# Kernel tuning notes

Hardware: AMD Instinct MI355X
Metric: run time of the kernel (lower is better)

## Reference

```python
import math
import jax
import jax.numpy as jnp
import numpy as np

N_IMG = 8
A = 3
H = 100
W = 100
STRIDE = 16
IMG = 1600
PRE_NMS_TOP_N = 2000
POST_NMS_TOP_N = 1000
NMS_THRESH = 0.7
MIN_SIZE = 0
BBOX_XFORM_CLIP = math.log(1000.0 / 16.0)


def setup_inputs() -> dict:
    key = jax.random.key(0)
    k1, k2 = jax.random.split(key)
    objectness = jax.random.normal(k1, (N_IMG, A, H, W), jnp.float32)
    box_regression = jax.random.normal(k2, (N_IMG, A * 4, H, W), jnp.float32) * 0.5
    # Grid anchors, flattened in (H, W, A) order to match objectness.permute(0,2,3,1)
    cy = (jnp.arange(H, dtype=jnp.float32) + 0.5) * STRIDE  # [H]
    cx = (jnp.arange(W, dtype=jnp.float32) + 0.5) * STRIDE  # [W]
    half = jnp.array([64.0, 128.0, 256.0], jnp.float32) / 2.0  # [A]
    cy = cy[:, None, None]  # [H,1,1]
    cx = cx[None, :, None]  # [1,W,1]
    s = half[None, None, :]  # [1,1,A]
    x1, y1, x2, y2 = jnp.broadcast_arrays(cx - s, cy - s, cx + s, cy + s)
    anc = jnp.stack([x1, y1, x2, y2], axis=-1).reshape(-1, 4)  # [H*W*A, 4]
    anchors = jnp.broadcast_to(anc[None], (N_IMG, H * W * A, 4)).copy()
    return {
        "objectness": objectness,
        "box_regression": box_regression,
        "anchors": anchors,
        "image_height": IMG,
        "image_width": IMG,
    }


def _decode(deltas, boxes):
    # BoxCoder(weights=(1,1,1,1)).decode with TO_REMOVE=1
    widths = boxes[..., 2] - boxes[..., 0] + 1.0
    heights = boxes[..., 3] - boxes[..., 1] + 1.0
    ctr_x = boxes[..., 0] + 0.5 * widths
    ctr_y = boxes[..., 1] + 0.5 * heights
    dx, dy = deltas[..., 0], deltas[..., 1]
    dw = jnp.minimum(deltas[..., 2], BBOX_XFORM_CLIP)
    dh = jnp.minimum(deltas[..., 3], BBOX_XFORM_CLIP)
    pcx = dx * widths + ctr_x
    pcy = dy * heights + ctr_y
    pw = jnp.exp(dw) * widths
    ph = jnp.exp(dh) * heights
    return jnp.stack(
        [pcx - 0.5 * pw, pcy - 0.5 * ph, pcx + 0.5 * pw - 1.0, pcy + 0.5 * ph - 1.0],
        axis=-1,
    )


def _nms_keep(boxes, valid, thresh):
    # boxes [n,4] sorted by descending score; valid: pre-filter mask.
    n = boxes.shape[0]
    x1, y1, x2, y2 = boxes[:, 0], boxes[:, 1], boxes[:, 2], boxes[:, 3]
    areas = (x2 - x1 + 1.0) * (y2 - y1 + 1.0)
    xx1 = jnp.maximum(x1[:, None], x1[None, :])
    yy1 = jnp.maximum(y1[:, None], y1[None, :])
    xx2 = jnp.minimum(x2[:, None], x2[None, :])
    yy2 = jnp.minimum(y2[:, None], y2[None, :])
    inter = jnp.maximum(xx2 - xx1 + 1.0, 0.0) * jnp.maximum(yy2 - yy1 + 1.0, 0.0)
    iou = inter / (areas[:, None] + areas[None, :] - inter)
    idx = jnp.arange(n)

    def body(i, keep):
        sup = keep[i] & (iou[i] > thresh) & (idx > i)
        return keep & ~sup

    return jax.lax.fori_loop(0, n, body, valid)


def _forward(objectness, box_regression, anchors, image_height, image_width):
    N, A_, H_, W_ = objectness.shape
    scores = jax.nn.sigmoid(objectness.transpose(0, 2, 3, 1).reshape(N, -1))  # [N, A*H*W]
    deltas = (
        box_regression.reshape(N, A_, 4, H_, W_)
        .transpose(0, 3, 4, 1, 2)
        .reshape(N, -1, 4)
    )
    pre = min(PRE_NMS_TOP_N, scores.shape[1])
    top_scores, top_idx = jax.lax.top_k(scores, pre)  # sorted descending
    deltas = jnp.take_along_axis(deltas, top_idx[:, :, None], axis=1)
    anc = jnp.take_along_axis(anchors, top_idx[:, :, None], axis=1)
    props = _decode(deltas, anc)  # [N, pre, 4]
    # clip to image (fact = 1)
    xs = jnp.clip(props[..., 0::2], 0.0, image_width - 1.0)
    ys = jnp.clip(props[..., 1::2], 0.0, image_height - 1.0)
    props = jnp.stack([xs[..., 0], ys[..., 0], xs[..., 1], ys[..., 1]], axis=-1)
    # filter small / out-of-image-center boxes
    ws = props[..., 2] - props[..., 0] + 1.0
    hs = props[..., 3] - props[..., 1] + 1.0
    xc = props[..., 0] + ws / 2.0
    yc = props[..., 1] + hs / 2.0
    valid = (ws >= MIN_SIZE) & (hs >= MIN_SIZE) & (xc < image_width) & (yc < image_height)
    keep = jax.vmap(lambda b, v: _nms_keep(b, v, NMS_THRESH))(props, valid)

    def _select(b, s, k):
        # compact kept boxes (already score-sorted) into fixed-size output
        rank = jnp.cumsum(k) - 1
        tgt = jnp.where(k & (rank < POST_NMS_TOP_N), rank, POST_NMS_TOP_N)
        ob = jnp.zeros((POST_NMS_TOP_N + 1, 4), b.dtype).at[tgt].set(b)[:POST_NMS_TOP_N]
        os = jnp.zeros((POST_NMS_TOP_N + 1,), s.dtype).at[tgt].set(s)[:POST_NMS_TOP_N]
        ov = jnp.arange(POST_NMS_TOP_N) < jnp.minimum(jnp.sum(k), POST_NMS_TOP_N)
        return ob, os, ov

    return jax.vmap(_select)(props, top_scores, keep)


def reference(objectness, box_regression, anchors, image_height, image_width):
    # Returns (boxes [N,post,4], objectness scores [N,post], valid mask [N,post])
    return _forward(objectness, box_regression, anchors, image_height, image_width)
```

## Files before the change

### kernel.cpp

```cpp
#include <hip/hip_runtime.h>
#include <math.h>
#include <stdint.h>

#define NIMG   8
#define NA     30000
#define PRE_N  2000
#define POST_N 1000
#define NMS_TH 0.7f
#define DCLIP  4.135166556742356f
#define IMGF   1600.0f
#define IMGM1  1599.0f
#define CAND_MAX 4096


__global__ __launch_bounds__(1024) void topk_decode(
    const float* __restrict__ obj, const float* __restrict__ breg,
    float* __restrict__ wsBoxes, float* __restrict__ wsScores,
    int* __restrict__ wsValid)
{
    const int n    = blockIdx.x;
    const int tid  = threadIdx.x;
    const int lane = tid & 63;
    const int wid  = tid >> 6;

    __shared__ unsigned int   hist[4096];
    __shared__ unsigned short sufx[4096];
    __shared__ uint64_t       grp[CAND_MAX];
    __shared__ unsigned int   wsum[16];
    __shared__ unsigned int   sbstar;

    for (int b = tid; b < 4096; b += 1024) hist[b] = 0u;
    __syncthreads();

    const float* objn = obj + n * NA;

    for (int j = tid; j < NA; j += 1024) {
        unsigned int u = __float_as_uint(objn[j]);
        unsigned int k = (u & 0x80000000u) ? ~u : (u | 0x80000000u);
        atomicAdd(&hist[k >> 20], 1u);
    }
    __syncthreads();

    unsigned int c0 = hist[tid*4+0], c1 = hist[tid*4+1],
                 c2 = hist[tid*4+2], c3 = hist[tid*4+3];
    unsigned int p = c0 + c1 + c2 + c3;
    unsigned int s = p;
    #pragma unroll
    for (int off = 1; off < 64; off <<= 1) {
        unsigned int v = __shfl_down(s, off);
        if (lane + off < 64) s += v;
    }
    if (lane == 0) wsum[wid] = s;
    __syncthreads();
    unsigned int wafter = 0;
    for (int w = wid + 1; w < 16; ++w) wafter += wsum[w];
    unsigned int after = (s - p) + wafter;
    {
        unsigned int S3 = after + c3;
        unsigned int S2 = S3 + c2;
        unsigned int S1 = S2 + c1;
        unsigned int S0 = S1 + c0;
        if (S3 >= PRE_N && after < PRE_N) { sbstar = tid*4+3; }
        if (S2 >= PRE_N && S3    < PRE_N) { sbstar = tid*4+2; }
        if (S1 >= PRE_N && S2    < PRE_N) { sbstar = tid*4+1; }
        if (S0 >= PRE_N && S1    < PRE_N) { sbstar = tid*4+0; }
        sufx[tid*4+0] = (unsigned short)S1;
        sufx[tid*4+1] = (unsigned short)S2;
        sufx[tid*4+2] = (unsigned short)S3;
        sufx[tid*4+3] = (unsigned short)after;
    }
    hist[tid*4+0] = 0u; hist[tid*4+1] = 0u;
    hist[tid*4+2] = 0u; hist[tid*4+3] = 0u;
    __syncthreads();
    const unsigned int bstar = sbstar;

    for (int j = tid; j < NA; j += 1024) {
        unsigned int u = __float_as_uint(objn[j]);
        unsigned int k = (u & 0x80000000u) ? ~u : (u | 0x80000000u);
        unsigned int b = k >> 20;
        if (b < bstar) continue;
        int a = j / 10000, t = j - a * 10000;
        uint64_t key = (((uint64_t)(~k)) << 32) | (unsigned int)(t * 3 + a);
        unsigned int slot = (unsigned int)sufx[b] + atomicAdd(&hist[b], 1u);
        if (slot < CAND_MAX) grp[slot] = key;
    }
    __syncthreads();

    const unsigned int total =
        min((unsigned int)sufx[bstar] + hist[bstar], (unsigned int)CAND_MAX);

    for (unsigned int slot = tid; slot < total; slot += 1024) {
        const uint64_t key = grp[slot];
        const unsigned int hi = (unsigned int)(key >> 32);
        const unsigned int b  = 4095u - (hi >> 20);
        const unsigned int gbeg = sufx[b];
        const unsigned int gend =
            min(gbeg + hist[b], (unsigned int)CAND_MAX);
        unsigned int rank = gbeg;
        unsigned int g = gbeg;
        for (; g + 8u <= gend; g += 8u) {
            uint64_t v0 = grp[g+0], v1 = grp[g+1], v2 = grp[g+2], v3 = grp[g+3];
            uint64_t v4 = grp[g+4], v5 = grp[g+5], v6 = grp[g+6], v7 = grp[g+7];
            unsigned int r0 = (v0 < key) ? 1u : 0u;
            r0 += (v1 < key) ? 1u : 0u;
            r0 += (v2 < key) ? 1u : 0u;
            r0 += (v3 < key) ? 1u : 0u;
            r0 += (v4 < key) ? 1u : 0u;
            r0 += (v5 < key) ? 1u : 0u;
            r0 += (v6 < key) ? 1u : 0u;
            r0 += (v7 < key) ? 1u : 0u;
            rank += r0;
        }
        for (; g < gend; ++g)
            rank += (grp[g] < key) ? 1u : 0u;
        if (rank >= PRE_N) continue;

        unsigned int idx = (unsigned int)key;
        unsigned int k   = ~hi;
        unsigned int u   = (k & 0x80000000u) ? (k & 0x7fffffffu) : ~k;
        float logit = __uint_as_float(u);
        float score = 1.0f / (1.0f + expf(-logit));

        int a = idx % 3, t = idx / 3, w = t % 100, h = t / 100;
        const float* bp = breg + n*120000 + (a*4)*10000 + t;
        float dx = bp[0], dy = bp[10000], dw = bp[20000], dh = bp[30000];

        float half = (a == 0) ? 32.0f : ((a == 1) ? 64.0f : 128.0f);
        float cx = w * 16.0f + 8.0f, cy = h * 16.0f + 8.0f;
        float x1 = cx - half, y1 = cy - half, x2 = cx + half, y2 = cy + half;
        float wd = x2 - x1 + 1.0f, hg = y2 - y1 + 1.0f;
        float cxr = x1 + 0.5f * wd, cyr = y1 + 0.5f * hg;
        dw = fminf(dw, DCLIP); dh = fminf(dh, DCLIP);
        float pcx = dx * wd + cxr, pcy = dy * hg + cyr;
        float pw = expf(dw) * wd, ph = expf(dh) * hg;
        float px1 = pcx - 0.5f * pw, py1 = pcy - 0.5f * ph;
        float px2 = pcx + 0.5f * pw - 1.0f, py2 = pcy + 0.5f * ph - 1.0f;
        px1 = fminf(fmaxf(px1, 0.0f), IMGM1);
        px2 = fminf(fmaxf(px2, 0.0f), IMGM1);
        py1 = fminf(fmaxf(py1, 0.0f), IMGM1);
        py2 = fminf(fmaxf(py2, 0.0f), IMGM1);
        float wss = px2 - px1 + 1.0f, hss = py2 - py1 + 1.0f;
        float xc = px1 + wss * 0.5f, yc = py1 + hss * 0.5f;
        int valid = (wss >= 0.0f) && (hss >= 0.0f) && (xc < IMGF) && (yc < IMGF);

        ((float4*)wsBoxes)[n * PRE_N + (int)rank] = make_float4(px1, py1, px2, py2);
        wsScores[n * PRE_N + (int)rank] = score;
        wsValid [n * PRE_N + (int)rank] = valid;
    }
}

__global__ __launch_bounds__(512) void nms_mask(
    const float* __restrict__ wsBoxes, uint64_t* __restrict__ mask)
{
    const int blk  = blockIdx.x;
    const int n    = blk >> 5;
    const int i_t  = blk & 31;
    const int tid  = threadIdx.x;
    const int lane = tid & 63;
    const int wv   = tid >> 6;

    __shared__ uint64_t tile[64 * 33];

    for (int idx = tid; idx < 64 * 33; idx += 512) tile[idx] = 0ull;
    __syncthreads();

    const int r = i_t * 64 + lane;
    float4 rb = (r < PRE_N) ? ((const float4*)wsBoxes)[n * PRE_N + r]
                            : make_float4(0.f, 0.f, 0.f, 0.f);
    float ra = (rb.z - rb.x + 1.0f) * (rb.w - rb.y + 1.0f);

    for (int j_t = i_t + wv; j_t < 32; j_t += 8) {
        const int j = j_t * 64 + lane;
        float4 cb = (j < PRE_N) ? ((const float4*)wsBoxes)[n * PRE_N + j]
                                : make_float4(3e30f, 3e30f, 3e30f, 3e30f);
        float ca = (cb.z - cb.x + 1.0f) * (cb.w - cb.y + 1.0f);
        const uint64_t jmask = (j_t == 31) ? 0xFFFFull : ~0ull;
        const bool diag = (j_t == i_t);
        uint64_t myword = 0ull;

        #pragma unroll
        for (int c = 0; c < 64; ++c) {
            float rx1 = __int_as_float(__builtin_amdgcn_readlane(__float_as_int(rb.x), c));
            float ry1 = __int_as_float(__builtin_amdgcn_readlane(__float_as_int(rb.y), c));
            float rx2 = __int_as_float(__builtin_amdgcn_readlane(__float_as_int(rb.z), c));
            float ry2 = __int_as_float(__builtin_amdgcn_readlane(__float_as_int(rb.w), c));
            float rar = __int_as_float(__builtin_amdgcn_readlane(__float_as_int(ra), c));
            float xx1 = fmaxf(rx1, cb.x), yy1 = fmaxf(ry1, cb.y);
            float xx2 = fminf(rx2, cb.z), yy2 = fminf(ry2, cb.w);
            float ww = fmaxf(xx2 - xx1 + 1.0f, 0.0f);
            float hh = fmaxf(yy2 - yy1 + 1.0f, 0.0f);
            float inter = ww * hh;
            float denom = rar + ca - inter;
            unsigned long long bits = __ballot(inter > NMS_TH * denom) & jmask;
            if (diag) bits &= (c == 63) ? 0ull : ((~0ull) << (c + 1));
            if (lane == c) myword = bits;
        }
        tile[lane * 33 + j_t] = myword;
    }
    __syncthreads();

    uint64_t* mrow = mask + ((size_t)n * PRE_N + (size_t)i_t * 64) * 32;
    const int cmax = (i_t == 31) ? 16 : 64;
    for (int idx = tid; idx < cmax * 32; idx += 512) {
        const int rr = idx >> 5, w = idx & 31;
        mrow[idx] = tile[rr * 33 + w];
    }
}

#define SL(n,b) \
    "global_load_dword v" #n ", %[voff], %[sbase]\n\t" \
    "v_add_u32 %[voff], 0x100, %[voff]\n\t"

#define SS(n,b) \
    "s_waitcnt vmcnt(63)\n\t" \
    "v_readlane_b32 %[t], v" #n ", %[lw]\n\t" \
    "s_bitcmp1_b32 %[win], " #b "\n\t" \
    "s_cselect_b32 %[m], 0, -1\n\t" \
    "s_sub_i32 %[kept], %[kept], %[m]\n\t" \
    "s_and_b32 %[t], %[t], %[m]\n\t" \
    "s_or_b32 %[win], %[win], %[t]\n\t" \
    "v_and_b32 v" #n ", %[m], v" #n "\n\t" \
    "v_or_b32 %[rem], %[rem], v" #n "\n\t" \
    "global_load_dword v" #n ", %[voff], %[sbase]\n\t" \
    "v_add_u32 %[voff], 0x100, %[voff]\n\t"

#define SN(n,b,w) \
    "s_waitcnt vmcnt(" #w ")\n\t" \
    "v_readlane_b32 %[t], v" #n ", %[lw]\n\t" \
    "s_bitcmp1_b32 %[win], " #b "\n\t" \
    "s_cselect_b32 %[m], 0, -1\n\t" \
    "s_sub_i32 %[kept], %[kept], %[m]\n\t" \
    "s_and_b32 %[t], %[t], %[m]\n\t" \
    "s_or_b32 %[win], %[win], %[t]\n\t" \
    "v_and_b32 v" #n ", %[m], v" #n "\n\t" \
    "v_or_b32 %[rem], %[rem], v" #n "\n\t"

#define SWIN \
    "s_add_u32 %[lw], %[lw], 1\n\t" \
    "v_readlane_b32 %[t], %[rem], %[lw]\n\t" \
    "s_mov_b32 %[win], %[t]\n\t"

#define ROW_A(M) M(64,0) M(65,1) M(66,2) M(67,3) M(68,4) M(69,5) M(70,6) M(71,7) \
    M(72,8) M(73,9) M(74,10) M(75,11) M(76,12) M(77,13) M(78,14) M(79,15) \
    M(80,16) M(81,17) M(82,18) M(83,19) M(84,20) M(85,21) M(86,22) M(87,23) \
    M(88,24) M(89,25) M(90,26) M(91,27) M(92,28) M(93,29) M(94,30) M(95,31)
#define ROW_B(M) M(96,0) M(97,1) M(98,2) M(99,3) M(100,4) M(101,5) M(102,6) M(103,7) \
    M(104,8) M(105,9) M(106,10) M(107,11) M(108,12) M(109,13) M(110,14) M(111,15) \
    M(112,16) M(113,17) M(114,18) M(115,19) M(116,20) M(117,21) M(118,22) M(119,23) \
    M(120,24) M(121,25) M(122,26) M(123,27) M(124,28) M(125,29) M(126,30) M(127,31)

__global__ __launch_bounds__(256) void nms_scan_select(
    const float* __restrict__ wsBoxes, const float* __restrict__ wsScores,
    const int* __restrict__ wsValid, const uint64_t* __restrict__ mask,
    float* __restrict__ out)
{
    const int n   = blockIdx.x;
    const int tid = threadIdx.x;

    __shared__ __align__(8) unsigned char invb[256];
    __shared__ unsigned int keepw32[64];
    __shared__ int sscan[256];

    unsigned int byte = 0xFFu;
    if (tid < PRE_N / 8) {
        byte = 0u;
        for (int q = 0; q < 8; ++q)
            byte |= (wsValid[n * PRE_N + tid * 8 + q] ? 0u : 1u) << q;
    }
    invb[tid] = (unsigned char)byte;
    __syncthreads();

    if (tid < 64) {
        unsigned int rem = ((const unsigned int*)invb)[tid];
        unsigned long long sbase =
            (unsigned long long)(const void*)(mask + (size_t)n * PRE_N * 32);
        unsigned int voff = (unsigned int)(tid * 4);
        int win_, m_, t_, lw_, kept_, cnt_;

        asm volatile(
            "s_waitcnt vmcnt(0) lgkmcnt(0)\n\t"
            "s_mov_b32 %[kept], 0\n\t"
            "s_mov_b32 %[lw], 0\n\t"
            ROW_A(SL) ROW_B(SL)
            "v_readlane_b32 %[t], %[rem], %[lw]\n\t"
            "s_mov_b32 %[win], %[t]\n\t"
            "s_mov_b32 %[cnt], 30\n\t"
            "Lnms_%=:\n\t"
            ROW_A(SS)
            SWIN
            ROW_B(SS)
            SWIN
            "s_cmp_ge_i32 %[kept], 0x3e8\n\t"
            "s_cbranch_scc1 Lend_%=\n\t"
            "s_sub_u32 %[cnt], %[cnt], 1\n\t"
            "s_cmp_lg_u32 %[cnt], 0\n\t"
            "s_cbranch_scc1 Lnms_%=\n\t"
            SS(64,0) SS(65,1) SS(66,2) SS(67,3) SS(68,4) SS(69,5) SS(70,6) SS(71,7)
            SS(72,8) SS(73,9) SS(74,10) SS(75,11) SS(76,12) SS(77,13) SS(78,14) SS(79,15)
            SN(80,16,63) SN(81,17,62) SN(82,18,61) SN(83,19,60)
            SN(84,20,59) SN(85,21,58) SN(86,22,57) SN(87,23,56)
            SN(88,24,55) SN(89,25,54) SN(90,26,53) SN(91,27,52)
            SN(92,28,51) SN(93,29,50) SN(94,30,49) SN(95,31,48)
            SWIN
            SN(96,0,47) SN(97,1,46) SN(98,2,45) SN(99,3,44)
            SN(100,4,43) SN(101,5,42) SN(102,6,41) SN(103,7,40)
            SN(104,8,39) SN(105,9,38) SN(106,10,37) SN(107,11,36)
            SN(108,12,35) SN(109,13,34) SN(110,14,33) SN(111,15,32)
            SN(112,16,31) SN(113,17,30) SN(114,18,29) SN(115,19,28)
            SN(116,20,27) SN(117,21,26) SN(118,22,25) SN(119,23,24)
            SN(120,24,23) SN(121,25,22) SN(122,26,21) SN(123,27,20)
            SN(124,28,19) SN(125,29,18) SN(126,30,17) SN(127,31,16)
            SWIN
            SN(64,0,15) SN(65,1,14) SN(66,2,13) SN(67,3,12)
            SN(68,4,11) SN(69,5,10) SN(70,6,9) SN(71,7,8)
            SN(72,8,7) SN(73,9,6) SN(74,10,5) SN(75,11,4)
            SN(76,12,3) SN(77,13,2) SN(78,14,1) SN(79,15,0)
            "Lend_%=:\n\t"
            "s_waitcnt vmcnt(0)\n\t"
            : [rem]"+v"(rem), [voff]"+v"(voff),
              [win]"=&s"(win_), [m]"=&s"(m_), [t]"=&s"(t_),
              [lw]"=&s"(lw_), [kept]"=&s"(kept_), [cnt]"=&s"(cnt_)
            : [sbase]"s"(sbase)
            : "scc", "vcc", "memory",
              "v64","v65","v66","v67","v68","v69","v70","v71",
              "v72","v73","v74","v75","v76","v77","v78","v79",
              "v80","v81","v82","v83","v84","v85","v86","v87",
              "v88","v89","v90","v91","v92","v93","v94","v95",
              "v96","v97","v98","v99","v100","v101","v102","v103",
              "v104","v105","v106","v107","v108","v109","v110","v111",
              "v112","v113","v114","v115","v116","v117","v118","v119",
              "v120","v121","v122","v123","v124","v125","v126","v127");

        keepw32[tid] = ~rem;
    }
    __syncthreads();

    int c[8]; const int base8 = tid * 8;
    int lsum = 0;
    for (int q = 0; q < 8; ++q) {
        const int i = base8 + q;
        c[q] = (i < PRE_N) ? (int)((keepw32[i >> 5] >> (i & 31)) & 1u) : 0;
        lsum += c[q];
    }
    sscan[tid] = lsum;
    __syncthreads();
    for (int off = 1; off < 256; off <<= 1) {
        int v = (tid >= off) ? sscan[tid - off] : 0;
        __syncthreads();
        sscan[tid] += v;
        __syncthreads();
    }
    const int excl  = sscan[tid] - lsum;
    const int total = sscan[255];

    float* ob  = out + n * POST_N * 4;
    float* osc = out + NIMG * POST_N * 4 + n * POST_N;
    float* ovd = out + NIMG * POST_N * 5 + n * POST_N;

    for (int i = tid; i < POST_N * 4; i += 256) ob[i] = 0.0f;
    for (int i = tid; i < POST_N; i += 256) osc[i] = 0.0f;
    const int lim = min(total, POST_N);
    for (int i = tid; i < POST_N; i += 256) ovd[i] = (i < lim) ? 1.0f : 0.0f;
    __syncthreads();

    int run = excl;
    for (int q = 0; q < 8; ++q) {
        const int i = base8 + q;
        if (i < PRE_N && c[q]) {
            if (run < POST_N) {
                float4 b = ((const float4*)wsBoxes)[n * PRE_N + i];
                ob[run * 4 + 0] = b.x;
                ob[run * 4 + 1] = b.y;
                ob[run * 4 + 2] = b.z;
                ob[run * 4 + 3] = b.w;
                osc[run] = wsScores[n * PRE_N + i];
            }
            run++;
        }
    }
}

extern "C" void kernel_launch(void* const* d_in, const int* in_sizes, int n_in,
                              void* d_out, int out_size, void* d_ws, size_t ws_size,
                              hipStream_t stream) {
    const float* obj  = (const float*)d_in[0];
    const float* breg = (const float*)d_in[1];
    float* ws        = (float*)d_ws;
    float* wsBoxes   = ws;
    float* wsScores  = ws + 64000;
    int*   wsValid   = (int*)(ws + 80000);
    uint64_t* wsMask = (uint64_t*)(ws + 96000);

    topk_decode<<<NIMG, 1024, 0, stream>>>(obj, breg, wsBoxes, wsScores, wsValid);
    nms_mask<<<NIMG * 32, 512, 0, stream>>>(wsBoxes, wsMask);
    nms_scan_select<<<NIMG, 256, 0, stream>>>(wsBoxes, wsScores, wsValid, wsMask,
                                              (float*)d_out);
}
```

Measured before the change: 176.2 us.

## Add second-level radix split for oversized histogram bins in top-k ranking

Bins holding more than 64 candidates are subdivided by a second 12-bit radix histogram and scatter into a secondary buffer, so each element's rank comes from comparing only within its small sub-bin instead of scanning the whole large bin. This targets the quadratic rank computation in dense bins near the top of normal-distributed logits. It adds extra shared memory (another histogram, suffix array and candidate buffer) and several block-wide barriers per large bin, which may lower occupancy and add serial overhead.

```diff
diff --git a/kernel.cpp b/kernel.cpp
--- a/kernel.cpp
+++ b/kernel.cpp
@@ -11,7 +11,46 @@
 #define IMGF   1600.0f
 #define IMGM1  1599.0f
 #define CAND_MAX 4096
-
+#define BIG_BIN  64
+
+
+__device__ __forceinline__ void decode_store(
+    uint64_t key, unsigned int rank, int n, const float* __restrict__ breg,
+    float* __restrict__ wsBoxes, float* __restrict__ wsScores,
+    int* __restrict__ wsValid)
+{
+    unsigned int idx = (unsigned int)key;
+    unsigned int k   = ~((unsigned int)(key >> 32));
+    unsigned int u   = (k & 0x80000000u) ? (k & 0x7fffffffu) : ~k;
+    float logit = __uint_as_float(u);
+    float score = 1.0f / (1.0f + expf(-logit));
+
+    int a = idx % 3, t = idx / 3, w = t % 100, h = t / 100;
+    const float* bp = breg + n*120000 + (a*4)*10000 + t;
+    float dx = bp[0], dy = bp[10000], dw = bp[20000], dh = bp[30000];
+
+    float half = (a == 0) ? 32.0f : ((a == 1) ? 64.0f : 128.0f);
+    float cx = w * 16.0f + 8.0f, cy = h * 16.0f + 8.0f;
+    float x1 = cx - half, y1 = cy - half, x2 = cx + half, y2 = cy + half;
+    float wd = x2 - x1 + 1.0f, hg = y2 - y1 + 1.0f;
+    float cxr = x1 + 0.5f * wd, cyr = y1 + 0.5f * hg;
+    dw = fminf(dw, DCLIP); dh = fminf(dh, DCLIP);
+    float pcx = dx * wd + cxr, pcy = dy * hg + cyr;
+    float pw = expf(dw) * wd, ph = expf(dh) * hg;
+    float px1 = pcx - 0.5f * pw, py1 = pcy - 0.5f * ph;
+    float px2 = pcx + 0.5f * pw - 1.0f, py2 = pcy + 0.5f * ph - 1.0f;
+    px1 = fminf(fmaxf(px1, 0.0f), IMGM1);
+    px2 = fminf(fmaxf(px2, 0.0f), IMGM1);
+    py1 = fminf(fmaxf(py1, 0.0f), IMGM1);
+    py2 = fminf(fmaxf(py2, 0.0f), IMGM1);
+    float wss = px2 - px1 + 1.0f, hss = py2 - py1 + 1.0f;
+    float xc = px1 + wss * 0.5f, yc = py1 + hss * 0.5f;
+    int valid = (wss >= 0.0f) && (hss >= 0.0f) && (xc < IMGF) && (yc < IMGF);
+
+    ((float4*)wsBoxes)[n * PRE_N + (int)rank] = make_float4(px1, py1, px2, py2);
+    wsScores[n * PRE_N + (int)rank] = score;
+    wsValid [n * PRE_N + (int)rank] = valid;
+}
 
 __global__ __launch_bounds__(1024) void topk_decode(
     const float* __restrict__ obj, const float* __restrict__ breg,
@@ -26,10 +65,16 @@
     __shared__ unsigned int   hist[4096];
     __shared__ unsigned short sufx[4096];
     __shared__ uint64_t       grp[CAND_MAX];
+    __shared__ unsigned int   hist2[4096];
+    __shared__ unsigned short sufx2[4096];
+    __shared__ uint64_t       grp2[CAND_MAX];
     __shared__ unsigned int   wsum[16];
     __shared__ unsigned int   sbstar;
+    __shared__ int            lbin[64];
+    __shared__ unsigned int   lbcnt;
 
     for (int b = tid; b < 4096; b += 1024) hist[b] = 0u;
+    if (tid == 0) lbcnt = 0u;
     __syncthreads();
 
     const float* objn = obj + n * NA;
@@ -69,10 +114,22 @@
         sufx[tid*4+2] = (unsigned short)S3;
         sufx[tid*4+3] = (unsigned short)after;
     }
-    hist[tid*4+0] = 0u; hist[tid*4+1] = 0u;
-    hist[tid*4+2] = 0u; hist[tid*4+3] = 0u;
     __syncthreads();
     const unsigned int bstar = sbstar;
+
+    {
+        const unsigned int cc[4] = {c0, c1, c2, c3};
+        #pragma unroll
+        for (int q = 0; q < 4; ++q) {
+            const unsigned int b = (unsigned int)(tid*4 + q);
+            hist[b] = 0u;
+            if (b >= bstar && cc[q] > (unsigned int)BIG_BIN) {
+                unsigned int pos = atomicAdd(&lbcnt, 1u);
+                if (pos < 64u) lbin[pos] = (int)b;
+            }
+        }
+    }
+    __syncthreads();
 
     for (int j = tid; j < NA; j += 1024) {
         unsigned int u = __float_as_uint(objn[j]);
@@ -88,14 +145,79 @@
 
     const unsigned int total =
         min((unsigned int)sufx[bstar] + hist[bstar], (unsigned int)CAND_MAX);
+    const unsigned int nlb = min(lbcnt, 64u);
+
+    for (unsigned int li = 0; li < nlb; ++li) {
+        const unsigned int L    = (unsigned int)lbin[li];
+        const unsigned int gbeg = sufx[L];
+        const unsigned int gend = min(gbeg + hist[L], (unsigned int)CAND_MAX);
+        const unsigned int m    = gend - gbeg;
+
+        for (int sb = tid; sb < 4096; sb += 1024) hist2[sb] = 0u;
+        __syncthreads();
+
+        for (unsigned int s2 = gbeg + tid; s2 < gend; s2 += 1024) {
+            unsigned int k = ~((unsigned int)(grp[s2] >> 32));
+            atomicAdd(&hist2[(k >> 8) & 0xfffu], 1u);
+        }
+        __syncthreads();
+
+        {
+            unsigned int d0 = hist2[tid*4+0], d1 = hist2[tid*4+1],
+                         d2 = hist2[tid*4+2], d3 = hist2[tid*4+3];
+            unsigned int pp = d0 + d1 + d2 + d3;
+            unsigned int ss = pp;
+            #pragma unroll
+            for (int off = 1; off < 64; off <<= 1) {
+                unsigned int v = __shfl_down(ss, off);
+                if (lane + off < 64) ss += v;
+            }
+            if (lane == 0) wsum[wid] = ss;
+            __syncthreads();
+            unsigned int wa = 0;
+            for (int w = wid + 1; w < 16; ++w) wa += wsum[w];
+            unsigned int af = (ss - pp) + wa;
+            sufx2[tid*4+0] = (unsigned short)(af + d3 + d2 + d1);
+            sufx2[tid*4+1] = (unsigned short)(af + d3 + d2);
+            sufx2[tid*4+2] = (unsigned short)(af + d3);
+            sufx2[tid*4+3] = (unsigned short)af;
+            hist2[tid*4+0] = 0u; hist2[tid*4+1] = 0u;
+            hist2[tid*4+2] = 0u; hist2[tid*4+3] = 0u;
+        }
+        __syncthreads();
+
+        for (unsigned int s2 = gbeg + tid; s2 < gend; s2 += 1024) {
+            uint64_t key = grp[s2];
+            unsigned int k  = ~((unsigned int)(key >> 32));
+            unsigned int sb = (k >> 8) & 0xfffu;
+            unsigned int d  = sufx2[sb] + atomicAdd(&hist2[sb], 1u);
+            grp2[d] = key;
+        }
+        __syncthreads();
+
+        for (unsigned int s2 = tid; s2 < m; s2 += 1024) {
+            uint64_t key = grp2[s2];
+            unsigned int k   = ~((unsigned int)(key >> 32));
+            unsigned int sb  = (k >> 8) & 0xfffu;
+            unsigned int b2  = sufx2[sb];
+            unsigned int e2  = b2 + hist2[sb];
+            unsigned int rank = gbeg + b2;
+            for (unsigned int g = b2; g < e2; ++g)
+                rank += (grp2[g] < key) ? 1u : 0u;
+            if (rank < PRE_N)
+                decode_store(key, rank, n, breg, wsBoxes, wsScores, wsValid);
+        }
+        __syncthreads();
+    }
 
     for (unsigned int slot = tid; slot < total; slot += 1024) {
         const uint64_t key = grp[slot];
         const unsigned int hi = (unsigned int)(key >> 32);
         const unsigned int b  = 4095u - (hi >> 20);
+        const unsigned int cntb = hist[b];
+        if (cntb > (unsigned int)BIG_BIN) continue;
         const unsigned int gbeg = sufx[b];
-        const unsigned int gend =
-            min(gbeg + hist[b], (unsigned int)CAND_MAX);
+        const unsigned int gend = min(gbeg + cntb, (unsigned int)CAND_MAX);
         unsigned int rank = gbeg;
         unsigned int g = gbeg;
         for (; g + 8u <= gend; g += 8u) {
@@ -114,38 +236,7 @@
         for (; g < gend; ++g)
             rank += (grp[g] < key) ? 1u : 0u;
         if (rank >= PRE_N) continue;
-
-        unsigned int idx = (unsigned int)key;
-        unsigned int k   = ~hi;
-        unsigned int u   = (k & 0x80000000u) ? (k & 0x7fffffffu) : ~k;
-        float logit = __uint_as_float(u);
-        float score = 1.0f / (1.0f + expf(-logit));
-
-        int a = idx % 3, t = idx / 3, w = t % 100, h = t / 100;
-        const float* bp = breg + n*120000 + (a*4)*10000 + t;
-        float dx = bp[0], dy = bp[10000], dw = bp[20000], dh = bp[30000];
-
-        float half = (a == 0) ? 32.0f : ((a == 1) ? 64.0f : 128.0f);
-        float cx = w * 16.0f + 8.0f, cy = h * 16.0f + 8.0f;
-        float x1 = cx - half, y1 = cy - half, x2 = cx + half, y2 = cy + half;
-        float wd = x2 - x1 + 1.0f, hg = y2 - y1 + 1.0f;
-        float cxr = x1 + 0.5f * wd, cyr = y1 + 0.5f * hg;
-        dw = fminf(dw, DCLIP); dh = fminf(dh, DCLIP);
-        float pcx = dx * wd + cxr, pcy = dy * hg + cyr;
-        float pw = expf(dw) * wd, ph = expf(dh) * hg;
-        float px1 = pcx - 0.5f * pw, py1 = pcy - 0.5f * ph;
-        float px2 = pcx + 0.5f * pw - 1.0f, py2 = pcy + 0.5f * ph - 1.0f;
-        px1 = fminf(fmaxf(px1, 0.0f), IMGM1);
-        px2 = fminf(fmaxf(px2, 0.0f), IMGM1);
-        py1 = fminf(fmaxf(py1, 0.0f), IMGM1);
-        py2 = fminf(fmaxf(py2, 0.0f), IMGM1);
-        float wss = px2 - px1 + 1.0f, hss = py2 - py1 + 1.0f;
-        float xc = px1 + wss * 0.5f, yc = py1 + hss * 0.5f;
-        int valid = (wss >= 0.0f) && (hss >= 0.0f) && (xc < IMGF) && (yc < IMGF);
-
-        ((float4*)wsBoxes)[n * PRE_N + (int)rank] = make_float4(px1, py1, px2, py2);
-        wsScores[n * PRE_N + (int)rank] = score;
-        wsValid [n * PRE_N + (int)rank] = valid;
+        decode_store(key, rank, n, breg, wsBoxes, wsScores, wsValid);
     }
 }
 
```

After: 178.5 us. About the same (+1.3%).

## Keep objectness in registers via float4 loads and replicate shared histograms

Applied to the files above, without the earlier changes.

The top-k kernel now loads each image's objectness once as float4 vectors held in registers and reuses them for both the histogram pass and the candidate scatter pass, instead of reading global memory twice. The histogram is split into four padded replicas, one per group of waves, to reduce atomic contention. Per-replica exclusive offsets are computed during the prefix scan so the scatter can take slots straight from atomics. The cost is more shared memory (four histogram copies) and more register pressure, which may reduce occupancy. Decode is moved into a helper function.

```diff
diff --git a/kernel.cpp b/kernel.cpp
--- a/kernel.cpp
+++ b/kernel.cpp
@@ -4,6 +4,7 @@
 
 #define NIMG   8
 #define NA     30000
+#define NQ4    7500
 #define PRE_N  2000
 #define POST_N 1000
 #define NMS_TH 0.7f
@@ -11,7 +12,51 @@
 #define IMGF   1600.0f
 #define IMGM1  1599.0f
 #define CAND_MAX 4096
-
+#define HPITCH 4104
+
+
+__device__ __forceinline__ void decode_store(
+    uint64_t key, unsigned int rank, int n, const float* __restrict__ breg,
+    float* __restrict__ wsBoxes, float* __restrict__ wsScores,
+    int* __restrict__ wsValid)
+{
+    unsigned int idx = (unsigned int)key;
+    unsigned int k   = ~((unsigned int)(key >> 32));
+    unsigned int u   = (k & 0x80000000u) ? (k & 0x7fffffffu) : ~k;
+    float logit = __uint_as_float(u);
+    float score = 1.0f / (1.0f + expf(-logit));
+
+    int a = idx % 3, t = idx / 3, w = t % 100, h = t / 100;
+    const float* bp = breg + n*120000 + (a*4)*10000 + t;
+    float dx = bp[0], dy = bp[10000], dw = bp[20000], dh = bp[30000];
+
+    float half = (a == 0) ? 32.0f : ((a == 1) ? 64.0f : 128.0f);
+    float cx = w * 16.0f + 8.0f, cy = h * 16.0f + 8.0f;
+    float x1 = cx - half, y1 = cy - half, x2 = cx + half, y2 = cy + half;
+    float wd = x2 - x1 + 1.0f, hg = y2 - y1 + 1.0f;
+    float cxr = x1 + 0.5f * wd, cyr = y1 + 0.5f * hg;
+    dw = fminf(dw, DCLIP); dh = fminf(dh, DCLIP);
+    float pcx = dx * wd + cxr, pcy = dy * hg + cyr;
+    float pw = expf(dw) * wd, ph = expf(dh) * hg;
+    float px1 = pcx - 0.5f * pw, py1 = pcy - 0.5f * ph;
+    float px2 = pcx + 0.5f * pw - 1.0f, py2 = pcy + 0.5f * ph - 1.0f;
+    px1 = fminf(fmaxf(px1, 0.0f), IMGM1);
+    px2 = fminf(fmaxf(px2, 0.0f), IMGM1);
+    py1 = fminf(fmaxf(py1, 0.0f), IMGM1);
+    py2 = fminf(fmaxf(py2, 0.0f), IMGM1);
+    float wss = px2 - px1 + 1.0f, hss = py2 - py1 + 1.0f;
+    float xc = px1 + wss * 0.5f, yc = py1 + hss * 0.5f;
+    int valid = (wss >= 0.0f) && (hss >= 0.0f) && (xc < IMGF) && (yc < IMGF);
+
+    ((float4*)wsBoxes)[n * PRE_N + (int)rank] = make_float4(px1, py1, px2, py2);
+    wsScores[n * PRE_N + (int)rank] = score;
+    wsValid [n * PRE_N + (int)rank] = valid;
+}
+
+__device__ __forceinline__ unsigned int keyof(float f) {
+    unsigned int u = __float_as_uint(f);
+    return (u & 0x80000000u) ? ~u : (u | 0x80000000u);
+}
 
 __global__ __launch_bounds__(1024) void topk_decode(
     const float* __restrict__ obj, const float* __restrict__ breg,
@@ -22,33 +67,48 @@
     const int tid  = threadIdx.x;
     const int lane = tid & 63;
     const int wid  = tid >> 6;
-
-    __shared__ unsigned int   hist[4096];
+    const int rep  = wid & 3;
+
+    __shared__ unsigned int   histf[4 * HPITCH];
     __shared__ unsigned short sufx[4096];
     __shared__ uint64_t       grp[CAND_MAX];
     __shared__ unsigned int   wsum[16];
     __shared__ unsigned int   sbstar;
 
-    for (int b = tid; b < 4096; b += 1024) hist[b] = 0u;
-    __syncthreads();
-
-    const float* objn = obj + n * NA;
-
-    for (int j = tid; j < NA; j += 1024) {
-        unsigned int u = __float_as_uint(objn[j]);
-        unsigned int k = (u & 0x80000000u) ? ~u : (u | 0x80000000u);
-        atomicAdd(&hist[k >> 20], 1u);
-    }
-    __syncthreads();
-
-    unsigned int c0 = hist[tid*4+0], c1 = hist[tid*4+1],
-                 c2 = hist[tid*4+2], c3 = hist[tid*4+3];
+    for (int b = tid; b < 4 * HPITCH; b += 1024) histf[b] = 0u;
+    __syncthreads();
+
+    const float4* obj4 = (const float4*)(obj + n * NA);
+    float4 v[8];
+    #pragma unroll
+    for (int kk = 0; kk < 7; ++kk) v[kk] = obj4[tid + kk * 1024];
+    v[7] = make_float4(0.f, 0.f, 0.f, 0.f);
+    if (tid < NQ4 - 7 * 1024) v[7] = obj4[tid + 7 * 1024];
+
+    #pragma unroll
+    for (int kk = 0; kk < 8; ++kk) {
+        if (kk == 7 && tid >= NQ4 - 7 * 1024) continue;
+        atomicAdd(&histf[rep * HPITCH + (keyof(v[kk].x) >> 20)], 1u);
+        atomicAdd(&histf[rep * HPITCH + (keyof(v[kk].y) >> 20)], 1u);
+        atomicAdd(&histf[rep * HPITCH + (keyof(v[kk].z) >> 20)], 1u);
+        atomicAdd(&histf[rep * HPITCH + (keyof(v[kk].w) >> 20)], 1u);
+    }
+    __syncthreads();
+
+    unsigned int c0, c1, c2, c3;
+    {
+        const int b0 = tid * 4;
+        c0 = histf[b0+0] + histf[HPITCH+b0+0] + histf[2*HPITCH+b0+0] + histf[3*HPITCH+b0+0];
+        c1 = histf[b0+1] + histf[HPITCH+b0+1] + histf[2*HPITCH+b0+1] + histf[3*HPITCH+b0+1];
+        c2 = histf[b0+2] + histf[HPITCH+b0+2] + histf[2*HPITCH+b0+2] + histf[3*HPITCH+b0+2];
+        c3 = histf[b0+3] + histf[HPITCH+b0+3] + histf[2*HPITCH+b0+3] + histf[3*HPITCH+b0+3];
+    }
     unsigned int p = c0 + c1 + c2 + c3;
     unsigned int s = p;
     #pragma unroll
     for (int off = 1; off < 64; off <<= 1) {
-        unsigned int v = __shfl_down(s, off);
-        if (lane + off < 64) s += v;
+        unsigned int vv = __shfl_down(s, off);
+        if (lane + off < 64) s += vv;
     }
     if (lane == 0) wsum[wid] = s;
     __syncthreads();
@@ -68,34 +128,49 @@
         sufx[tid*4+1] = (unsigned short)S2;
         sufx[tid*4+2] = (unsigned short)S3;
         sufx[tid*4+3] = (unsigned short)after;
-    }
-    hist[tid*4+0] = 0u; hist[tid*4+1] = 0u;
-    hist[tid*4+2] = 0u; hist[tid*4+3] = 0u;
+
+        const unsigned int st[4] = {S1, S2, S3, after};
+        #pragma unroll
+        for (int q = 0; q < 4; ++q) {
+            const int b = tid*4 + q;
+            unsigned int base = st[q];
+            #pragma unroll
+            for (int r = 0; r < 4; ++r) {
+                unsigned int c = histf[r * HPITCH + b];
+                histf[r * HPITCH + b] = base;
+                base += c;
+            }
+        }
+    }
     __syncthreads();
     const unsigned int bstar = sbstar;
 
-    for (int j = tid; j < NA; j += 1024) {
-        unsigned int u = __float_as_uint(objn[j]);
-        unsigned int k = (u & 0x80000000u) ? ~u : (u | 0x80000000u);
-        unsigned int b = k >> 20;
-        if (b < bstar) continue;
-        int a = j / 10000, t = j - a * 10000;
-        uint64_t key = (((uint64_t)(~k)) << 32) | (unsigned int)(t * 3 + a);
-        unsigned int slot = (unsigned int)sufx[b] + atomicAdd(&hist[b], 1u);
-        if (slot < CAND_MAX) grp[slot] = key;
-    }
-    __syncthreads();
-
-    const unsigned int total =
-        min((unsigned int)sufx[bstar] + hist[bstar], (unsigned int)CAND_MAX);
+    #pragma unroll
+    for (int kk = 0; kk < 8; ++kk) {
+        if (kk == 7 && tid >= NQ4 - 7 * 1024) continue;
+        const float fv[4] = {v[kk].x, v[kk].y, v[kk].z, v[kk].w};
+        #pragma unroll
+        for (int e = 0; e < 4; ++e) {
+            unsigned int k = keyof(fv[e]);
+            unsigned int b = k >> 20;
+            if (b < bstar) continue;
+            int j = (tid + kk * 1024) * 4 + e;
+            int a = j / 10000, t = j - a * 10000;
+            uint64_t key = (((uint64_t)(~k)) << 32) | (unsigned int)(t * 3 + a);
+            unsigned int slot = atomicAdd(&histf[rep * HPITCH + b], 1u);
+            if (slot < CAND_MAX) grp[slot] = key;
+        }
+    }
+    __syncthreads();
+
+    const unsigned int total = min(histf[3 * HPITCH + bstar], (unsigned int)CAND_MAX);
 
     for (unsigned int slot = tid; slot < total; slot += 1024) {
         const uint64_t key = grp[slot];
         const unsigned int hi = (unsigned int)(key >> 32);
         const unsigned int b  = 4095u - (hi >> 20);
         const unsigned int gbeg = sufx[b];
-        const unsigned int gend =
-            min(gbeg + hist[b], (unsigned int)CAND_MAX);
+        const unsigned int gend = min(histf[3 * HPITCH + b], (unsigned int)CAND_MAX);
         unsigned int rank = gbeg;
         unsigned int g = gbeg;
         for (; g + 8u <= gend; g += 8u) {
@@ -114,38 +189,7 @@
         for (; g < gend; ++g)
             rank += (grp[g] < key) ? 1u : 0u;
         if (rank >= PRE_N) continue;
-
-        unsigned int idx = (unsigned int)key;
-        unsigned int k   = ~hi;
-        unsigned int u   = (k & 0x80000000u) ? (k & 0x7fffffffu) : ~k;
-        float logit = __uint_as_float(u);
-        float score = 1.0f / (1.0f + expf(-logit));
-
-        int a = idx % 3, t = idx / 3, w = t % 100, h = t / 100;
-        const float* bp = breg + n*120000 + (a*4)*10000 + t;
-        float dx = bp[0], dy = bp[10000], dw = bp[20000], dh = bp[30000];
-
-        float half = (a == 0) ? 32.0f : ((a == 1) ? 64.0f : 128.0f);
-        float cx = w * 16.0f + 8.0f, cy = h * 16.0f + 8.0f;
-        float x1 = cx - half, y1 = cy - half, x2 = cx + half, y2 = cy + half;
-        float wd = x2 - x1 + 1.0f, hg = y2 - y1 + 1.0f;
-        float cxr = x1 + 0.5f * wd, cyr = y1 + 0.5f * hg;
-        dw = fminf(dw, DCLIP); dh = fminf(dh, DCLIP);
-        float pcx = dx * wd + cxr, pcy = dy * hg + cyr;
-        float pw = expf(dw) * wd, ph = expf(dh) * hg;
-        float px1 = pcx - 0.5f * pw, py1 = pcy - 0.5f * ph;
-        float px2 = pcx + 0.5f * pw - 1.0f, py2 = pcy + 0.5f * ph - 1.0f;
-        px1 = fminf(fmaxf(px1, 0.0f), IMGM1);
-        px2 = fminf(fmaxf(px2, 0.0f), IMGM1);
-        py1 = fminf(fmaxf(py1, 0.0f), IMGM1);
-        py2 = fminf(fmaxf(py2, 0.0f), IMGM1);
-        float wss = px2 - px1 + 1.0f, hss = py2 - py1 + 1.0f;
-        float xc = px1 + wss * 0.5f, yc = py1 + hss * 0.5f;
-        int valid = (wss >= 0.0f) && (hss >= 0.0f) && (xc < IMGF) && (yc < IMGF);
-
-        ((float4*)wsBoxes)[n * PRE_N + (int)rank] = make_float4(px1, py1, px2, py2);
-        wsScores[n * PRE_N + (int)rank] = score;
-        wsValid [n * PRE_N + (int)rank] = valid;
+        decode_store(key, rank, n, breg, wsBoxes, wsScores, wsValid);
     }
 }
 
```

Result: faster. 167.6 us (-4.9%).
